# Kernel optimization log

Hardware: AMD Instinct MI355X
Metric: run time of the kernel (lower is better)

Reference implementation:

```python
import jax, jax.numpy as jnp
import numpy as np

B, N = 4, 1024
D_MODEL, N_HEADS, D_HEAD, D_COORD = 512, 8, 64, 2


def setup_inputs() -> dict:
    key = jax.random.key(0)
    ks = jax.random.split(key, 8)
    sd = 1.0 / np.sqrt(D_MODEL)
    return {
        "x": jax.random.normal(ks[0], (B, N, D_MODEL), dtype=jnp.float32),
        "positions": jax.random.uniform(ks[1], (N, D_COORD), dtype=jnp.float32) * 32.0,
        "W_Q": jax.random.normal(ks[2], (D_MODEL, N_HEADS * D_HEAD), dtype=jnp.float32) * sd,
        "W_K": jax.random.normal(ks[3], (D_MODEL, N_HEADS * D_HEAD), dtype=jnp.float32) * sd,
        "W_V": jax.random.normal(ks[4], (D_MODEL, N_HEADS * D_HEAD), dtype=jnp.float32) * sd,
        "W_O": jax.random.normal(ks[5], (N_HEADS * D_HEAD, D_MODEL), dtype=jnp.float32) * sd,
        "U": jax.random.normal(ks[6], (N_HEADS, D_HEAD, D_HEAD), dtype=jnp.float32),
        "freqs": jax.random.normal(ks[7], (N_HEADS, D_HEAD // 2, D_COORD), dtype=jnp.float32),
    }


def reference(x, positions, W_Q, W_K, W_V, W_O, U, freqs):
    # x: (B,N,d_model); positions: (N,d_coord); U: (H,dh,dh); freqs: (H,m,d_coord)
    Bn, Nn, _ = x.shape
    H, dh, _ = U.shape
    m = dh // 2
    scale = (dh // 2) ** -0.5

    Q = (x @ W_Q).reshape(Bn, Nn, H, dh)
    K = (x @ W_K).reshape(Bn, Nn, H, dh)
    V = (x @ W_V).reshape(Bn, Nn, H, dh)

    # Active-subspace projector: Pi = qr(U)[0] @ qr(U)[0].T per head
    Uq = jax.vmap(lambda u: jnp.linalg.qr(u)[0])(U)              # (H,dh,dh)
    P = jnp.einsum('hde,hfe->hdf', Uq, Uq)                       # U U^T
    Qp = jnp.einsum('bnhd,hdf->bhnf', Q, P)                      # (B,H,N,dh)
    Kp = jnp.einsum('bnhd,hdf->bhnf', K, P)

    # Relative rotation: R_rel(r_j - r_i) is block-diag 2x2 rotations with
    # angle theta_ijm = freqs_m . (r_j - r_i) = a_jm - a_im (separable), so
    # q^T R(r_j-r_i) k = (R(a_i)q)^T (R(a_j)k)  -- exact RoPE identity.
    ang = jnp.einsum('nc,hmc->hnm', positions, freqs)            # (H,N,m)
    c = jnp.cos(ang)[None]                                       # (1,H,N,m)
    s = jnp.sin(ang)[None]

    def rot(v):  # v: (B,H,N,dh) -> rotated (even, odd) halves (B,H,N,m)
        ve, vo = v[..., ::2], v[..., 1::2]
        return ve * c - vo * s, ve * s + vo * c

    qe, qo = rot(Qp)
    ke, ko = rot(Kp)
    scores = (jnp.einsum('bhim,bhjm->bhij', qe, ke)
              + jnp.einsum('bhim,bhjm->bhij', qo, ko)) * scale   # (B,H,N,N)
    w = jax.nn.softmax(scores, axis=-1)
    out = jnp.einsum('bhij,bjhd->bihd', w, V).reshape(Bn, Nn, H * dh)
    return out @ W_O
```

## Files before the change

### kernel.cpp

```cpp
#include <hip/hip_runtime.h>
#include <hip/hip_bf16.h>
#include <math.h>

#define NBATCH 4
#define NSEQ   1024
#define DMODEL 512
#define NH     8
#define DH     64
#define MROWS  (NBATCH*NSEQ)
#define MHALF  (DH/2)

typedef __attribute__((ext_vector_type(8))) short bf16x8;
typedef __attribute__((ext_vector_type(4))) float floatx4;

__device__ __forceinline__ uint f2bf2(float lo, float hi) {
    union { __hip_bfloat162 h; uint u; } v;
    v.h = __float22bfloat162_rn(make_float2(lo, hi));
    return v.u;
}

__global__ __launch_bounds__(256) void prep_kernel(
    const float* __restrict__ pos, const float* __restrict__ freqs,
    const float* __restrict__ x,
    const float* __restrict__ Wq, const float* __restrict__ Wk,
    const float* __restrict__ Wv, const float* __restrict__ Wo,
    float* __restrict__ cosT, float* __restrict__ sinT,
    ushort* __restrict__ xb, ushort* __restrict__ Wt)
{
    __shared__ float T[64][65];
    const int bid = blockIdx.x;
    const int tid = threadIdx.x;

    if (bid < 1024) {
        int idx = bid * 256 + tid;
        int m = idx & 31;
        int n = (idx >> 5) & 1023;
        int h = idx >> 15;
        float a = pos[n*2+0] * freqs[(h*MHALF+m)*2+0]
                + pos[n*2+1] * freqs[(h*MHALF+m)*2+1];
        cosT[idx] = cosf(a);
        sinT[idx] = sinf(a);
    } else if (bid < 2048) {
        int idx = ((bid - 1024) * 256 + tid) * 8;
        float4 a = *(const float4*)&x[idx];
        float4 b = *(const float4*)&x[idx+4];
        uint4 pk;
        pk.x = f2bf2(a.x, a.y);
        pk.y = f2bf2(a.z, a.w);
        pk.z = f2bf2(b.x, b.y);
        pk.w = f2bf2(b.z, b.w);
        *(uint4*)&xb[idx] = pk;
    } else {
        int b2 = bid - 2048;
        int n0g = (b2 & 31) * 64;
        int k0  = (b2 >> 5) * 64;
        int mat = n0g >> 9;
        const float* W = (mat == 0) ? Wq : ((mat == 1) ? Wk : ((mat == 2) ? Wv : Wo));
        int n0 = n0g & 511;
        int c = tid & 63, r = tid >> 6;
        #pragma unroll
        for (int i = 0; i < 16; i++)
            T[r + i*4][c] = W[(k0 + r + i*4) * DMODEL + n0 + c];
        __syncthreads();
        int nl = tid >> 2;
        int kg = tid & 3;
        #pragma unroll
        for (int g = 0; g < 4; g++) {
            int kl = kg * 16 + g * 4;
            uint2 pk;
            pk.x = f2bf2(T[kl+0][nl], T[kl+1][nl]);
            pk.y = f2bf2(T[kl+2][nl], T[kl+3][nl]);
            *(uint2*)&Wt[(size_t)(n0g + nl) * DMODEL + k0 + kl] = pk;
        }
    }
}

__global__ __launch_bounds__(256) void qkv_gemm(
    const ushort* __restrict__ xb, const ushort* __restrict__ Wt,
    const float* __restrict__ cosT, const float* __restrict__ sinT,
    ushort* __restrict__ Qb, ushort* __restrict__ Kb, ushort* __restrict__ Vt)
{
    __shared__ __align__(16) ushort AB[2 * 64 * 72];
    ushort* As = AB;
    ushort* Bs = AB + 64 * 72;
    float (*Cs)[65] = (float(*)[65])AB;

    const int cb = blockIdx.x;
    const int rb = blockIdx.y;
    const int mat = cb >> 3;
    const int c0 = (cb & 7) * 64;
    const int r0 = rb * 64;
    const int ng0 = mat * 512 + c0;

    const int tid = threadIdx.x;
    const int w = tid >> 6, l = tid & 63;
    const int lr = l & 15, lg = l >> 4;

    const int srow = tid >> 2;
    const int scol = (tid & 3) * 16;

    floatx4 acc[4];
    #pragma unroll
    for (int nt = 0; nt < 4; nt++) acc[nt] = (floatx4){0.f,0.f,0.f,0.f};

    const ushort* pa = &xb[(size_t)(r0 + srow) * DMODEL + scol];
    const ushort* pb = &Wt[(size_t)(ng0 + srow) * DMODEL + scol];
    uint4 ra0 = *(const uint4*)pa;
    uint4 ra1 = *(const uint4*)(pa + 8);
    uint4 rb0 = *(const uint4*)pb;
    uint4 rb1 = *(const uint4*)(pb + 8);

    for (int k0 = 0; k0 < DMODEL; k0 += 64) {
        __syncthreads();
        *(uint4*)&As[srow*72 + scol]     = ra0;
        *(uint4*)&As[srow*72 + scol + 8] = ra1;
        *(uint4*)&Bs[srow*72 + scol]     = rb0;
        *(uint4*)&Bs[srow*72 + scol + 8] = rb1;
        __syncthreads();

        if (k0 + 64 < DMODEL) {
            const ushort* na = &xb[(size_t)(r0 + srow) * DMODEL + k0 + 64 + scol];
            const ushort* nb = &Wt[(size_t)(ng0 + srow) * DMODEL + k0 + 64 + scol];
            ra0 = *(const uint4*)na;
            ra1 = *(const uint4*)(na + 8);
            rb0 = *(const uint4*)nb;
            rb1 = *(const uint4*)(nb + 8);
        }

        #pragma unroll
        for (int ks = 0; ks < 2; ks++) {
            bf16x8 af = *(const bf16x8*)&As[(16*w + lr)*72 + ks*32 + lg*8];
            #pragma unroll
            for (int nt = 0; nt < 4; nt++) {
                bf16x8 bf = *(const bf16x8*)&Bs[(nt*16 + lr)*72 + ks*32 + lg*8];
                acc[nt] = __builtin_amdgcn_mfma_f32_16x16x32_bf16(af, bf, acc[nt], 0, 0, 0);
            }
        }
    }

    __syncthreads();
    #pragma unroll
    for (int nt = 0; nt < 4; nt++)
        #pragma unroll
        for (int r = 0; r < 4; r++)
            Cs[16*w + lg*4 + r][nt*16 + lr] = acc[nt][r];
    __syncthreads();

    const int tx = tid & 15, ty = tid >> 4;
    const int dbase = tx * 4;
    const int head = c0 >> 6;

    if (mat == 2) {
        int rowbase = r0 + ty * 4;
        int b = rowbase >> 10, n0 = rowbase & 1023;
        size_t vbase = (size_t)(b * NH + head) * DH;
        #pragma unroll
        for (int j = 0; j < 4; j++) {
            uint2 pk;
            pk.x = f2bf2(Cs[ty*4 + 0][tx*4 + j], Cs[ty*4 + 1][tx*4 + j]);
            pk.y = f2bf2(Cs[ty*4 + 2][tx*4 + j], Cs[ty*4 + 3][tx*4 + j]);
            *(uint2*)&Vt[(vbase + dbase + j) * NSEQ + n0] = pk;
        }
    } else {
        ushort* dst = (mat == 0) ? Qb : Kb;
        const float qs2 = (mat == 0) ? 0.17677669529663687f : 1.0f;
        #pragma unroll
        for (int i = 0; i < 4; i++) {
            int row = r0 + ty * 4 + i;
            int b = row >> 10, n = row & 1023;
            float v[4];
            #pragma unroll
            for (int p = 0; p < 2; p++) {
                int de = dbase + 2 * p;
                int m = de >> 1;
                float c = cosT[(head * NSEQ + n) * MHALF + m] * qs2;
                float s = sinT[(head * NSEQ + n) * MHALF + m] * qs2;
                float ve = Cs[ty*4 + i][tx*4 + 2*p];
                float vo = Cs[ty*4 + i][tx*4 + 2*p + 1];
                v[2*p]     = ve * c - vo * s;
                v[2*p + 1] = ve * s + vo * c;
            }
            uint2 pk;
            pk.x = f2bf2(v[0], v[1]);
            pk.y = f2bf2(v[2], v[3]);
            *(uint2*)&dst[((size_t)(b * NH + head) * NSEQ + n) * DH + dbase] = pk;
        }
    }
}

__global__ __launch_bounds__(256, 4) void attn_kernel(
    const ushort* __restrict__ Qb, const ushort* __restrict__ Kb,
    const ushort* __restrict__ Vt, ushort* __restrict__ Obb)
{
    __shared__ __align__(16) ushort S[2*64*72 + 32*72];
    ushort* Ks = S;
    ushort* Vs = S + 64*72;
    ushort* Ps = S + 2*64*72;

    const int tid = threadIdx.x;
    const int w = tid >> 6, l = tid & 63;
    const int lr = l & 15, lg = l >> 4;
    const int qs = w & 1;
    const int jh = w >> 1;
    const int bh = blockIdx.y, q0 = blockIdx.x * 32;

    const ushort* Qg = Qb + (size_t)bh * NSEQ * DH;
    const ushort* Kg = Kb + (size_t)bh * NSEQ * DH;
    const ushort* Vg = Vt + (size_t)bh * DH * NSEQ;

    bf16x8 qf[2];
    #pragma unroll
    for (int ks = 0; ks < 2; ks++)
        qf[ks] = *(const bf16x8*)(Qg + (size_t)(q0 + 16*qs + lr) * DH + ks*32 + lg*8);

    floatx4 ot[4];
    #pragma unroll
    for (int i = 0; i < 4; i++) ot[i] = (floatx4){0.f, 0.f, 0.f, 0.f};
    float l_lane = 0.f;

    const int sr = tid >> 2;
    const int sc = (tid & 3) * 16;

    const ushort* kp = Kg + (size_t)sr * DH + sc;
    uint4 ka  = *(const uint4*)kp;
    uint4 kb2 = *(const uint4*)(kp + 8);
    const ushort* vp = Vg + (size_t)sr * NSEQ + sc;
    uint4 va  = *(const uint4*)vp;
    uint4 vb2 = *(const uint4*)(vp + 8);

    for (int jt = 0; jt < 16; jt++) {
        __syncthreads();
        *(uint4*)&Ks[sr*72 + sc]     = ka;
        *(uint4*)&Ks[sr*72 + sc + 8] = kb2;
        *(uint4*)&Vs[sr*72 + sc]     = va;
        *(uint4*)&Vs[sr*72 + sc + 8] = vb2;
        __syncthreads();

        if (jt < 15) {
            const ushort* kn = Kg + (size_t)((jt+1)*64 + sr) * DH + sc;
            ka  = *(const uint4*)kn;
            kb2 = *(const uint4*)(kn + 8);
            const ushort* vn = Vg + (size_t)sr * NSEQ + (jt+1)*64 + sc;
            va  = *(const uint4*)vn;
            vb2 = *(const uint4*)(vn + 8);
        }

        #pragma unroll
        for (int jm2 = 0; jm2 < 2; jm2++) {
            const int jm = jh*2 + jm2;
            floatx4 acc = (floatx4){0.f, 0.f, 0.f, 0.f};
            #pragma unroll
            for (int ks = 0; ks < 2; ks++) {
                bf16x8 af = *(const bf16x8*)&Ks[(jm*16 + lr)*72 + ks*32 + lg*8];
                acc = __builtin_amdgcn_mfma_f32_16x16x32_bf16(af, qf[ks], acc, 0, 0, 0);
            }
            float p0 = __expf(acc[0]);
            float p1 = __expf(acc[1]);
            float p2 = __expf(acc[2]);
            float p3 = __expf(acc[3]);
            l_lane += (p0 + p1) + (p2 + p3);
            uint2 pk;
            pk.x = f2bf2(p0, p1);
            pk.y = f2bf2(p2, p3);
            *(uint2*)&Ps[(16*qs + lr)*72 + jm*16 + lg*4] = pk;
        }

        {
            bf16x8 pf = *(const bf16x8*)&Ps[(16*qs + lr)*72 + jh*32 + lg*8];
            #pragma unroll
            for (int dt = 0; dt < 4; dt++) {
                bf16x8 af = *(const bf16x8*)&Vs[(dt*16 + lr)*72 + jh*32 + lg*8];
                ot[dt] = __builtin_amdgcn_mfma_f32_16x16x32_bf16(af, pf, ot[dt], 0, 0, 0);
            }
        }
    }

    l_lane += __shfl_xor(l_lane, 16, 64);
    l_lane += __shfl_xor(l_lane, 32, 64);

    __syncthreads();
    float* Os = (float*)S;
    float* Ls = (float*)(S + 5120);
    if (w >= 2) {
        #pragma unroll
        for (int dt = 0; dt < 4; dt++)
            *(float4*)&Os[(qs*64 + l)*20 + dt*4] = *(float4*)&ot[dt];
        if (lg == 0) Ls[qs*16 + lr] = l_lane;
    }
    __syncthreads();
    if (w < 2) {
        float lsum = l_lane + Ls[qs*16 + lr];
        float inv = 1.f / lsum;
        int n = q0 + 16*qs + lr;
        size_t obase = ((size_t)bh * NSEQ + n) * DH;
        #pragma unroll
        for (int dt = 0; dt < 4; dt++) {
            float4 p = *(const float4*)&Os[(qs*64 + l)*20 + dt*4];
            uint2 pk;
            pk.x = f2bf2((ot[dt][0] + p.x) * inv, (ot[dt][1] + p.y) * inv);
            pk.y = f2bf2((ot[dt][2] + p.z) * inv, (ot[dt][3] + p.w) * inv);
            *(uint2*)&Obb[obase + dt*16 + lg*4] = pk;
        }
    }
}

__global__ __launch_bounds__(256) void out_gemm(
    const ushort* __restrict__ Obb, const ushort* __restrict__ Wt,
    float* __restrict__ out)
{
    __shared__ __align__(16) ushort AB[2 * 64 * 72];
    ushort* As = AB;
    ushort* Bs = AB + 64 * 72;
    float (*Cs)[65] = (float(*)[65])AB;

    const int cb = blockIdx.x;
    const int rb = blockIdx.y;
    const int c0 = cb * 64, r0 = rb * 64;

    const int tid = threadIdx.x;
    const int w = tid >> 6, l = tid & 63;
    const int lr = l & 15, lg = l >> 4;
    const int srow = tid >> 2;
    const int scol = (tid & 3) * 16;

    const int arow = r0 + srow;
    const int b = arow >> 10, n = arow & 1023;

    floatx4 acc[4];
    #pragma unroll
    for (int nt = 0; nt < 4; nt++) acc[nt] = (floatx4){0.f,0.f,0.f,0.f};

    #define A_ADDR(K0) (&Obb[((size_t)(b*NH + ((K0) >> 6)) * NSEQ + n) * DH + scol])

    const ushort* pb0 = &Wt[(size_t)(1536 + c0 + srow) * DMODEL + scol];
    uint4 ra0 = *(const uint4*)A_ADDR(0);
    uint4 ra1 = *(const uint4*)(A_ADDR(0) + 8);
    uint4 rb0 = *(const uint4*)pb0;
    uint4 rb1 = *(const uint4*)(pb0 + 8);

    for (int k0 = 0; k0 < DMODEL; k0 += 64) {
        __syncthreads();
        *(uint4*)&As[srow*72 + scol]     = ra0;
        *(uint4*)&As[srow*72 + scol + 8] = ra1;
        *(uint4*)&Bs[srow*72 + scol]     = rb0;
        *(uint4*)&Bs[srow*72 + scol + 8] = rb1;
        __syncthreads();

        if (k0 + 64 < DMODEL) {
            const ushort* na = A_ADDR(k0 + 64);
            const ushort* nb = &Wt[(size_t)(1536 + c0 + srow) * DMODEL + (k0 + 64) + scol];
            ra0 = *(const uint4*)na;
            ra1 = *(const uint4*)(na + 8);
            rb0 = *(const uint4*)nb;
            rb1 = *(const uint4*)(nb + 8);
        }

        #pragma unroll
        for (int ks = 0; ks < 2; ks++) {
            bf16x8 af = *(const bf16x8*)&As[(16*w + lr)*72 + ks*32 + lg*8];
            #pragma unroll
            for (int nt = 0; nt < 4; nt++) {
                bf16x8 bf = *(const bf16x8*)&Bs[(nt*16 + lr)*72 + ks*32 + lg*8];
                acc[nt] = __builtin_amdgcn_mfma_f32_16x16x32_bf16(af, bf, acc[nt], 0, 0, 0);
            }
        }
    }
    #undef A_ADDR

    __syncthreads();
    #pragma unroll
    for (int nt = 0; nt < 4; nt++)
        #pragma unroll
        for (int r = 0; r < 4; r++)
            Cs[16*w + lg*4 + r][nt*16 + lr] = acc[nt][r];
    __syncthreads();

    const int tx = tid & 15, ty = tid >> 4;
    #pragma unroll
    for (int i = 0; i < 4; i++) {
        float4 o;
        o.x = Cs[ty*4 + i][tx*4 + 0];
        o.y = Cs[ty*4 + i][tx*4 + 1];
        o.z = Cs[ty*4 + i][tx*4 + 2];
        o.w = Cs[ty*4 + i][tx*4 + 3];
        *(float4*)&out[(size_t)(r0 + ty*4 + i) * DMODEL + c0 + tx*4] = o;
    }
}

extern "C" void kernel_launch(void* const* d_in, const int* in_sizes, int n_in,
                              void* d_out, int out_size, void* d_ws, size_t ws_size,
                              hipStream_t stream) {
    const float* x         = (const float*)d_in[0];
    const float* positions = (const float*)d_in[1];
    const float* Wq        = (const float*)d_in[2];
    const float* Wk        = (const float*)d_in[3];
    const float* Wv        = (const float*)d_in[4];
    const float* Wo        = (const float*)d_in[5];
    const float* freqs     = (const float*)d_in[7];
    float* out = (float*)d_out;

    float*  ws    = (float*)d_ws;
    float*  cosT  = ws;
    float*  sinT  = cosT + NH*NSEQ*MHALF;
    ushort* xb    = (ushort*)(sinT + NH*NSEQ*MHALF);
    ushort* Wt    = xb + (size_t)MROWS*DMODEL;
    ushort* Qb    = Wt + (size_t)2048*DMODEL;
    ushort* Kb    = Qb + (size_t)NBATCH*NH*NSEQ*DH;
    ushort* Vt    = Kb + (size_t)NBATCH*NH*NSEQ*DH;
    ushort* Obb   = Vt + (size_t)NBATCH*NH*NSEQ*DH;

    prep_kernel<<<dim3(2304), 256, 0, stream>>>(positions, freqs, x, Wq, Wk, Wv, Wo,
                                                cosT, sinT, xb, Wt);
    qkv_gemm<<<dim3(24, 64), 256, 0, stream>>>(xb, Wt, cosT, sinT, Qb, Kb, Vt);
    attn_kernel<<<dim3(32, 32), 256, 0, stream>>>(Qb, Kb, Vt, Obb);
    out_gemm<<<dim3(8, 64), 256, 0, stream>>>(Obb, Wt, out);
}
```

Baseline: 122.4 us.

## Widen QKV GEMM tile to 64x128 with 2x2 warp layout

The QKV projection GEMM now computes a 64x128 output tile per block instead of 64x64, with each warp owning a 32x64 sub-tile (two A fragments reused across four B fragments). This halves the grid and improves LDS/register reuse of loaded fragments per MFMA, reducing shared-memory reads per flop. The epilogue is reworked to handle two heads per block and 8 rows per thread. Fewer blocks (768) may reduce occupancy/tail balance, and more accumulators raise register pressure.

Measured after the change: 121.1 us. No clear change (-1.1%).

```diff
diff --git a/kernel.cpp b/kernel.cpp
--- a/kernel.cpp
+++ b/kernel.cpp
@@ -80,110 +80,129 @@
     const float* __restrict__ cosT, const float* __restrict__ sinT,
     ushort* __restrict__ Qb, ushort* __restrict__ Kb, ushort* __restrict__ Vt)
 {
-    __shared__ __align__(16) ushort AB[2 * 64 * 72];
-    ushort* As = AB;
-    ushort* Bs = AB + 64 * 72;
-    float (*Cs)[65] = (float(*)[65])AB;
+    __shared__ __align__(16) ushort S[16896];
+    ushort* As = S;
+    ushort* Bs = S + 64*72;
+    float (*Cs)[132] = (float(*)[132])S;
 
     const int cb = blockIdx.x;
     const int rb = blockIdx.y;
-    const int mat = cb >> 3;
-    const int c0 = (cb & 7) * 64;
+    const int mat = cb >> 2;
+    const int c0 = (cb & 3) * 128;
     const int r0 = rb * 64;
     const int ng0 = mat * 512 + c0;
 
     const int tid = threadIdx.x;
     const int w = tid >> 6, l = tid & 63;
     const int lr = l & 15, lg = l >> 4;
-
-    const int srow = tid >> 2;
-    const int scol = (tid & 3) * 16;
-
-    floatx4 acc[4];
-    #pragma unroll
-    for (int nt = 0; nt < 4; nt++) acc[nt] = (floatx4){0.f,0.f,0.f,0.f};
-
-    const ushort* pa = &xb[(size_t)(r0 + srow) * DMODEL + scol];
-    const ushort* pb = &Wt[(size_t)(ng0 + srow) * DMODEL + scol];
+    const int wr = w & 1;
+    const int wc = w >> 1;
+
+    const int arow = tid >> 2;
+    const int acol = (tid & 3) * 16;
+    const int brow = tid >> 1;
+    const int bcol = (tid & 1) * 32;
+
+    floatx4 acc[2][4];
+    #pragma unroll
+    for (int mi = 0; mi < 2; mi++)
+        #pragma unroll
+        for (int nt = 0; nt < 4; nt++) acc[mi][nt] = (floatx4){0.f,0.f,0.f,0.f};
+
+    const ushort* pa = &xb[(size_t)(r0 + arow) * DMODEL + acol];
+    const ushort* pb = &Wt[(size_t)(ng0 + brow) * DMODEL + bcol];
     uint4 ra0 = *(const uint4*)pa;
     uint4 ra1 = *(const uint4*)(pa + 8);
     uint4 rb0 = *(const uint4*)pb;
     uint4 rb1 = *(const uint4*)(pb + 8);
+    uint4 rb2 = *(const uint4*)(pb + 16);
+    uint4 rb3 = *(const uint4*)(pb + 24);
 
     for (int k0 = 0; k0 < DMODEL; k0 += 64) {
         __syncthreads();
-        *(uint4*)&As[srow*72 + scol]     = ra0;
-        *(uint4*)&As[srow*72 + scol + 8] = ra1;
-        *(uint4*)&Bs[srow*72 + scol]     = rb0;
-        *(uint4*)&Bs[srow*72 + scol + 8] = rb1;
+        *(uint4*)&As[arow*72 + acol]     = ra0;
+        *(uint4*)&As[arow*72 + acol + 8] = ra1;
+        *(uint4*)&Bs[brow*72 + bcol]      = rb0;
+        *(uint4*)&Bs[brow*72 + bcol + 8]  = rb1;
+        *(uint4*)&Bs[brow*72 + bcol + 16] = rb2;
+        *(uint4*)&Bs[brow*72 + bcol + 24] = rb3;
         __syncthreads();
 
         if (k0 + 64 < DMODEL) {
-            const ushort* na = &xb[(size_t)(r0 + srow) * DMODEL + k0 + 64 + scol];
-            const ushort* nb = &Wt[(size_t)(ng0 + srow) * DMODEL + k0 + 64 + scol];
+            const ushort* na = &xb[(size_t)(r0 + arow) * DMODEL + k0 + 64 + acol];
+            const ushort* nb = &Wt[(size_t)(ng0 + brow) * DMODEL + k0 + 64 + bcol];
             ra0 = *(const uint4*)na;
             ra1 = *(const uint4*)(na + 8);
             rb0 = *(const uint4*)nb;
             rb1 = *(const uint4*)(nb + 8);
+            rb2 = *(const uint4*)(nb + 16);
+            rb3 = *(const uint4*)(nb + 24);
         }
 
         #pragma unroll
         for (int ks = 0; ks < 2; ks++) {
-            bf16x8 af = *(const bf16x8*)&As[(16*w + lr)*72 + ks*32 + lg*8];
+            bf16x8 af0 = *(const bf16x8*)&As[(wr*32 +  0 + lr)*72 + ks*32 + lg*8];
+            bf16x8 af1 = *(const bf16x8*)&As[(wr*32 + 16 + lr)*72 + ks*32 + lg*8];
             #pragma unroll
             for (int nt = 0; nt < 4; nt++) {
-                bf16x8 bf = *(const bf16x8*)&Bs[(nt*16 + lr)*72 + ks*32 + lg*8];
-                acc[nt] = __builtin_amdgcn_mfma_f32_16x16x32_bf16(af, bf, acc[nt], 0, 0, 0);
+                bf16x8 bf = *(const bf16x8*)&Bs[(wc*64 + nt*16 + lr)*72 + ks*32 + lg*8];
+                acc[0][nt] = __builtin_amdgcn_mfma_f32_16x16x32_bf16(af0, bf, acc[0][nt], 0, 0, 0);
+                acc[1][nt] = __builtin_amdgcn_mfma_f32_16x16x32_bf16(af1, bf, acc[1][nt], 0, 0, 0);
             }
         }
     }
 
     __syncthreads();
     #pragma unroll
-    for (int nt = 0; nt < 4; nt++)
-        #pragma unroll
-        for (int r = 0; r < 4; r++)
-            Cs[16*w + lg*4 + r][nt*16 + lr] = acc[nt][r];
-    __syncthreads();
-
-    const int tx = tid & 15, ty = tid >> 4;
-    const int dbase = tx * 4;
-    const int head = c0 >> 6;
+    for (int mi = 0; mi < 2; mi++)
+        #pragma unroll
+        for (int nt = 0; nt < 4; nt++)
+            #pragma unroll
+            for (int r = 0; r < 4; r++)
+                Cs[wr*32 + mi*16 + lg*4 + r][wc*64 + nt*16 + lr] = acc[mi][nt][r];
+    __syncthreads();
+
+    const int tx = tid & 31, ty = tid >> 5;
+    const int dloc = tx * 4;
+    const int head = (c0 + dloc) >> 6;
+    const int dh = (c0 + dloc) & 63;
 
     if (mat == 2) {
-        int rowbase = r0 + ty * 4;
+        int rowbase = r0 + ty * 8;
         int b = rowbase >> 10, n0 = rowbase & 1023;
-        size_t vbase = (size_t)(b * NH + head) * DH;
         #pragma unroll
         for (int j = 0; j < 4; j++) {
-            uint2 pk;
-            pk.x = f2bf2(Cs[ty*4 + 0][tx*4 + j], Cs[ty*4 + 1][tx*4 + j]);
-            pk.y = f2bf2(Cs[ty*4 + 2][tx*4 + j], Cs[ty*4 + 3][tx*4 + j]);
-            *(uint2*)&Vt[(vbase + dbase + j) * NSEQ + n0] = pk;
+            size_t base = ((size_t)(b * NH + head) * DH + dh + j) * NSEQ + n0;
+            uint2 p1, p2;
+            p1.x = f2bf2(Cs[ty*8 + 0][dloc + j], Cs[ty*8 + 1][dloc + j]);
+            p1.y = f2bf2(Cs[ty*8 + 2][dloc + j], Cs[ty*8 + 3][dloc + j]);
+            p2.x = f2bf2(Cs[ty*8 + 4][dloc + j], Cs[ty*8 + 5][dloc + j]);
+            p2.y = f2bf2(Cs[ty*8 + 6][dloc + j], Cs[ty*8 + 7][dloc + j]);
+            *(uint2*)&Vt[base]     = p1;
+            *(uint2*)&Vt[base + 4] = p2;
         }
     } else {
         ushort* dst = (mat == 0) ? Qb : Kb;
         const float qs2 = (mat == 0) ? 0.17677669529663687f : 1.0f;
         #pragma unroll
-        for (int i = 0; i < 4; i++) {
-            int row = r0 + ty * 4 + i;
+        for (int i = 0; i < 8; i++) {
+            int row = r0 + ty * 8 + i;
             int b = row >> 10, n = row & 1023;
             float v[4];
             #pragma unroll
             for (int p = 0; p < 2; p++) {
-                int de = dbase + 2 * p;
-                int m = de >> 1;
+                int m = (dh >> 1) + p;
                 float c = cosT[(head * NSEQ + n) * MHALF + m] * qs2;
                 float s = sinT[(head * NSEQ + n) * MHALF + m] * qs2;
-                float ve = Cs[ty*4 + i][tx*4 + 2*p];
-                float vo = Cs[ty*4 + i][tx*4 + 2*p + 1];
+                float ve = Cs[ty*8 + i][dloc + 2*p];
+                float vo = Cs[ty*8 + i][dloc + 2*p + 1];
                 v[2*p]     = ve * c - vo * s;
                 v[2*p + 1] = ve * s + vo * c;
             }
             uint2 pk;
             pk.x = f2bf2(v[0], v[1]);
             pk.y = f2bf2(v[2], v[3]);
-            *(uint2*)&dst[((size_t)(b * NH + head) * NSEQ + n) * DH + dbase] = pk;
+            *(uint2*)&dst[((size_t)(b * NH + head) * NSEQ + n) * DH + dh] = pk;
         }
     }
 }
@@ -411,7 +430,7 @@
 
     prep_kernel<<<dim3(2304), 256, 0, stream>>>(positions, freqs, x, Wq, Wk, Wv, Wo,
                                                 cosT, sinT, xb, Wt);
-    qkv_gemm<<<dim3(24, 64), 256, 0, stream>>>(xb, Wt, cosT, sinT, Qb, Kb, Vt);
+    qkv_gemm<<<dim3(12, 64), 256, 0, stream>>>(xb, Wt, cosT, sinT, Qb, Kb, Vt);
     attn_kernel<<<dim3(32, 32), 256, 0, stream>>>(Qb, Kb, Vt, Obb);
     out_gemm<<<dim3(8, 64), 256, 0, stream>>>(Obb, Wt, out);
 }
```
